# Kernel optimization log

Measured on AMD Instinct MI355X. Metric: run time of the kernel, lower is better.

Reference implementation:

```python
import jax, jax.numpy as jnp
import numpy as np

B, T, TC, C, CC, H = 2, 2048, 512, 1024, 512, 16
D = C // H  # head dim = 64


def setup_inputs() -> dict:
    key = jax.random.key(0)
    ks = jax.random.split(key, 18)
    w = lambda k, i, o: (jax.random.normal(k, (i, o), jnp.float32) / np.sqrt(i).astype(np.float32))
    return {
        "x": jax.random.normal(ks[0], (B, T, C), jnp.float32),
        "cross_input": jax.random.normal(ks[1], (B, TC, CC), jnp.float32),
        "Wk": w(ks[2], C, C),  "bk": jnp.zeros((C,), jnp.float32),
        "Wq": w(ks[3], C, C),  "bq": jnp.zeros((C,), jnp.float32),
        "Wv": w(ks[4], C, C),  "bv": jnp.zeros((C,), jnp.float32),
        "Wck": w(ks[5], CC, C), "bck": jnp.zeros((C,), jnp.float32),
        "Wcq": w(ks[6], C, C),  "bcq": jnp.zeros((C,), jnp.float32),
        "Wcv": w(ks[7], CC, C), "bcv": jnp.zeros((C,), jnp.float32),
        "Wp": w(ks[8], C, C),   "bp": jnp.zeros((C,), jnp.float32),
    }


def _heads(t):
    # [B, L, C] -> [B, H, L, D]
    b, l, _ = t.shape
    return t.reshape(b, l, H, D).transpose(0, 2, 1, 3)


def reference(x, cross_input, Wk, bk, Wq, bq, Wv, bv, Wck, bck, Wcq, bcq, Wcv, bcv, Wp, bp):
    scale = np.float32(1.0 / np.sqrt(D))
    q = _heads(x @ Wq + bq)
    k = _heads(x @ Wk + bk)
    v = _heads(x @ Wv + bv)
    # causal self-attention with materialized scores (faithful to original)
    att = jnp.einsum("bhqd,bhkd->bhqk", q, k) * scale
    causal = jnp.tril(jnp.ones((T, T), bool))
    att = jnp.where(causal[None, None], att, -jnp.inf)
    y = jnp.einsum("bhqk,bhkd->bhqd", jax.nn.softmax(att, axis=-1), v)
    # cross-attention (no mask)
    qc = _heads(x @ Wcq + bcq)
    kc = _heads(cross_input @ Wck + bck)
    vc = _heads(cross_input @ Wcv + bcv)
    attc = jnp.einsum("bhqd,bhkd->bhqk", qc, kc) * scale
    y = y + jnp.einsum("bhqk,bhkd->bhqd", jax.nn.softmax(attc, axis=-1), vc)
    # merge heads + output projection (dropout prob = 0 -> identity)
    y = y.transpose(0, 2, 1, 3).reshape(x.shape[0], T, C)
    return y @ Wp + bp
```

## Files before the change

kernel.cpp:

```cpp
#include <hip/hip_runtime.h>
#include <hip/hip_bf16.h>
#include <type_traits>

typedef __bf16 bf16;
typedef __bf16 bf16x8 __attribute__((ext_vector_type(8)));
typedef float floatx4 __attribute__((ext_vector_type(4)));

#if __has_builtin(__builtin_amdgcn_exp2f)
#define EXP2(x) __builtin_amdgcn_exp2f(x)
#else
#define EXP2(x) exp2f(x)
#endif

__device__ __forceinline__ void glds16(const bf16* g, bf16* l) {
  __builtin_amdgcn_global_load_lds((const __attribute__((address_space(1))) void*)g,
                                   (__attribute__((address_space(3))) void*)l, 16, 0, 0);
}

__device__ __forceinline__ unsigned pack_bf16(float a, float b) {
  unsigned short ua = __builtin_bit_cast(unsigned short, (bf16)a);
  unsigned short ub = __builtin_bit_cast(unsigned short, (bf16)b);
  return (unsigned)ua | ((unsigned)ub << 16);
}

struct PrepArgs {
  const float* x; const float* xc;
  bf16* xbf; bf16* xcbf;
  const float* b4[4];
  const float* bc[2];
  float* bias4; float* biasc;
  const float* W[7];
  bf16* WT[7];
};

__global__ __launch_bounds__(256) void prep_kernel(PrepArgs a) {
  __shared__ bf16 tsh[32][33];
  const int bx = blockIdx.x, tid = threadIdx.x;
  if (bx < 4096) {
    int i = bx * 256 + tid;
    float4 f = ((const float4*)a.x)[i];
    bf16 t[4] = {(bf16)f.x, (bf16)f.y, (bf16)f.z, (bf16)f.w};
    *(uint2*)&a.xbf[(long)i * 4] = *(const uint2*)t;
  } else if (bx < 4608) {
    int i = (bx - 4096) * 256 + tid;
    float4 f = ((const float4*)a.xc)[i];
    bf16 t[4] = {(bf16)f.x, (bf16)f.y, (bf16)f.z, (bf16)f.w};
    *(uint2*)&a.xcbf[(long)i * 4] = *(const uint2*)t;
  } else if (bx < 4632) {
    int lb = bx - 4608;
    if (lb < 16) { int i = lb * 256 + tid; a.bias4[i] = a.b4[i >> 10][i & 1023]; }
    else         { int i = (lb - 16) * 256 + tid; a.biasc[i] = a.bc[i >> 10][i & 1023]; }
  } else {
    int t = bx - 4632, w, R, bxw, byw;
    if (t < 5120) { w = t >> 10; R = 1024; int l = t & 1023; bxw = l & 31; byw = l >> 5; }
    else { int t2 = t - 5120; w = 5 + (t2 >> 9); R = 512; int l = t2 & 511; bxw = l & 31; byw = l >> 5; }
    const float* in = a.W[w];
    bf16* out = a.WT[w];
    int tx = tid & 31, ty = tid >> 5;
    int c = bxw * 32 + tx;
#pragma unroll
    for (int i = 0; i < 4; i++) {
      int r = byw * 32 + ty + i * 8;
      tsh[ty + i * 8][tx] = (bf16)in[(long)r * 1024 + c];
    }
    __syncthreads();
    int oc = byw * 32 + tx;
#pragma unroll
    for (int i = 0; i < 4; i++) {
      int orr = bxw * 32 + ty + i * 8;
      out[(long)orr * R + oc] = tsh[tx][ty + i * 8];
    }
  }
}

template <typename OutT>
__global__ __launch_bounds__(256, 3) void gemm128(const bf16* __restrict__ A,
                                                  const bf16* __restrict__ Bt,
                                                  const float* __restrict__ bias,
                                                  OutT* __restrict__ C,
                                                  int M, int N, int K, int ldc,
                                                  bf16* __restrict__ Vt,
                                                  int vcol0, int vcol1, int Lt, int tok_shift) {
  __shared__ alignas(16) bf16 As[128 * 32];
  __shared__ alignas(16) bf16 Bs[128 * 32];
  const int tid = threadIdx.x, wave = tid >> 6, lane = tid & 63;
  const int l16 = lane & 15, l4 = lane >> 4;
  const int wm = wave & 1, wn = wave >> 1;
  const int n0 = blockIdx.x * 128, m0 = blockIdx.y * 128;
  const int lrow = lane >> 2, lch = (lane & 3) * 8;

  floatx4 acc[4][4];
#pragma unroll
  for (int mt = 0; mt < 4; mt++)
#pragma unroll
    for (int nt = 0; nt < 4; nt++) acc[mt][nt] = (floatx4){0.f, 0.f, 0.f, 0.f};

  const bf16* Ag = A + (long)(m0 + wave * 32 + lrow) * K + lch;
  const bf16* Bg = Bt + (long)(n0 + wave * 32 + lrow) * K + lch;
  bf16* Al = &As[(wave * 32) * 32];
  bf16* Bl = &Bs[(wave * 32) * 32];

  for (int k0 = 0; k0 < K; k0 += 32) {
    __syncthreads();
    glds16(Ag + k0, Al);
    glds16(Ag + k0 + (long)16 * K, Al + 16 * 32);
    glds16(Bg + k0, Bl);
    glds16(Bg + k0 + (long)16 * K, Bl + 16 * 32);
    __syncthreads();
    bf16x8 a[4], b[4];
#pragma unroll
    for (int mt = 0; mt < 4; mt++) a[mt] = *(const bf16x8*)&As[(wm * 64 + mt * 16 + l16) * 32 + l4 * 8];
#pragma unroll
    for (int nt = 0; nt < 4; nt++) b[nt] = *(const bf16x8*)&Bs[(wn * 64 + nt * 16 + l16) * 32 + l4 * 8];
#pragma unroll
    for (int mt = 0; mt < 4; mt++)
#pragma unroll
      for (int nt = 0; nt < 4; nt++)
        acc[mt][nt] = __builtin_amdgcn_mfma_f32_16x16x32_bf16(a[mt], b[nt], acc[mt][nt], 0, 0, 0);
  }

  const bool vpath = (vcol0 >= 0) && (n0 >= vcol0) && (n0 < vcol1);
  if (!vpath) {
    const int coladj = (vcol0 >= 0 && n0 >= vcol1) ? (vcol1 - vcol0) : 0;
#pragma unroll
    for (int nt = 0; nt < 4; nt++) {
      int col = n0 + wn * 64 + nt * 16 + l16;
      float bv = bias[col];
#pragma unroll
      for (int mt = 0; mt < 4; mt++)
#pragma unroll
        for (int r = 0; r < 4; r++) {
          int row = m0 + wm * 64 + mt * 16 + l4 * 4 + r;
          float v = acc[mt][nt][r] + bv;
          if constexpr (std::is_same_v<OutT, float>) C[(long)row * ldc + col - coladj] = v;
          else                                       C[(long)row * ldc + col - coladj] = (bf16)v;
        }
    }
  } else {
#pragma unroll
    for (int nt = 0; nt < 4; nt++) {
      int col = n0 + wn * 64 + nt * 16 + l16;
      int c = col - vcol0, hh = c >> 6, dd = c & 63;
      float bv = bias[col];
#pragma unroll
      for (int mt = 0; mt < 4; mt++) {
        int t0 = m0 + wm * 64 + mt * 16 + l4 * 4;
        int bb = t0 >> tok_shift, t = t0 & ((1 << tok_shift) - 1);
        bf16 tmp[4];
#pragma unroll
        for (int r = 0; r < 4; r++) tmp[r] = (bf16)(acc[mt][nt][r] + bv);
        *(uint2*)&Vt[(((long)bb * 16 + hh) * 64 + dd) * Lt + t] = *(const uint2*)tmp;
      }
    }
  }
}

__global__ __launch_bounds__(256, 2) void attn_kernel(const bf16* __restrict__ QKQc,
                                                      const bf16* __restrict__ VtB,
                                                      const bf16* __restrict__ KcB,
                                                      const bf16* __restrict__ VctB,
                                                      bf16* __restrict__ Y) {
  __shared__ float2 Mbuf[4][4][16];
  __shared__ alignas(16) bf16 U[4 * 64 * 72];
  const int tid = threadIdx.x, w = tid >> 6, lane = tid & 63;
  const int l16 = lane & 15, l4 = lane >> 4;
  const int bh = blockIdx.x, h = bh & 15, b = bh >> 4;
  const int qt = 31 - (int)blockIdx.y;
  const int q0 = qt * 64;
  const int wk = w * 32;
  bf16* Pw = U + w * (64 * 48);
  const float NEG = -1e30f;

  float o_self[16];

  for (int phase = 0; phase < 2; phase++) {
    const bf16 *Qb, *Kb, *Vtb;
    int kstr, vtstr, nkt;
    if (phase == 0) {
      Qb = QKQc + (long)b * 2048 * 3072 + h * 64;
      Kb = Qb + 1024;                              kstr = 3072;
      Vtb = VtB + ((long)b * 16 + h) * 64 * 2048;  vtstr = 2048;
      nkt = (qt + 2) >> 1;
    } else {
      Qb = QKQc + (long)b * 2048 * 3072 + h * 64 + 2048;
      Kb = KcB + (long)b * 512 * 1024 + h * 64;    kstr = 1024;
      Vtb = VctB + ((long)b * 16 + h) * 64 * 512;  vtstr = 512;
      nkt = 4;
    }

    __syncthreads();

    bf16x8 qf[4][2];
#pragma unroll
    for (int qtt = 0; qtt < 4; qtt++) {
      const bf16* qp = Qb + (long)(q0 + qtt * 16 + l16) * 3072 + l4 * 8;
#pragma unroll
      for (int ds = 0; ds < 2; ds++) {
        bf16x8 v = *(const bf16x8*)(qp + ds * 32);
#pragma unroll
        for (int j = 0; j < 8; j++) v[j] = (bf16)((float)v[j] * 0.18033688f);
        qf[qtt][ds] = v;
      }
    }

    float m_i[4], l_i[4];
#pragma unroll
    for (int qtt = 0; qtt < 4; qtt++) { m_i[qtt] = NEG; l_i[qtt] = 0.f; }
    floatx4 oacc[4][4];
#pragma unroll
    for (int mtd = 0; mtd < 4; mtd++)
#pragma unroll
      for (int qtt = 0; qtt < 4; qtt++) oacc[mtd][qtt] = (floatx4){0.f, 0.f, 0.f, 0.f};

    bf16x8 kc[2][2], kn[2][2];
#pragma unroll
    for (int mt = 0; mt < 2; mt++)
#pragma unroll
      for (int ds = 0; ds < 2; ds++)
        kc[mt][ds] = *(const bf16x8*)(Kb + (long)(wk + mt * 16 + l16) * kstr + ds * 32 + l4 * 8);

    for (int kt = 0; kt < nkt; kt++) {
      const int kbase = kt * 128 + wk;
      bf16x8 vc[4];
#pragma unroll
      for (int mtd = 0; mtd < 4; mtd++)
        vc[mtd] = *(const bf16x8*)(Vtb + (long)(mtd * 16 + l16) * vtstr + kbase + l4 * 8);

      floatx4 sacc[2][4];
#pragma unroll
      for (int mt = 0; mt < 2; mt++)
#pragma unroll
        for (int qtt = 0; qtt < 4; qtt++) sacc[mt][qtt] = (floatx4){0.f, 0.f, 0.f, 0.f};
#pragma unroll
      for (int ds = 0; ds < 2; ds++)
#pragma unroll
        for (int mt = 0; mt < 2; mt++)
#pragma unroll
          for (int qtt = 0; qtt < 4; qtt++)
            sacc[mt][qtt] = __builtin_amdgcn_mfma_f32_16x16x32_bf16(kc[mt][ds], qf[qtt][ds], sacc[mt][qtt], 0, 0, 0);

      if (kt + 1 < nkt) {
        const int nb = kbase + 128;
#pragma unroll
        for (int mt = 0; mt < 2; mt++)
#pragma unroll
          for (int ds = 0; ds < 2; ds++)
            kn[mt][ds] = *(const bf16x8*)(Kb + (long)(nb + mt * 16 + l16) * kstr + ds * 32 + l4 * 8);
      }

      if (phase == 0 && kt == nkt - 1) {
#pragma unroll
        for (int mt = 0; mt < 2; mt++) {
          int keyb = kbase + mt * 16 + l4 * 4;
#pragma unroll
          for (int qtt = 0; qtt < 4; qtt++) {
            int q = q0 + qtt * 16 + l16;
#pragma unroll
            for (int r = 0; r < 4; r++)
              if (keyb + r > q) sacc[mt][qtt][r] = NEG;
          }
        }
      }

      float alpha[4];
      unsigned pd[4][2][2];
      int changed = 0;
#pragma unroll
      for (int qtt = 0; qtt < 4; qtt++) {
        float mx = fmaxf(fmaxf(fmaxf(sacc[0][qtt][0], sacc[0][qtt][1]), fmaxf(sacc[0][qtt][2], sacc[0][qtt][3])),
                         fmaxf(fmaxf(sacc[1][qtt][0], sacc[1][qtt][1]), fmaxf(sacc[1][qtt][2], sacc[1][qtt][3])));
        mx = fmaxf(mx, __shfl_xor(mx, 16));
        mx = fmaxf(mx, __shfl_xor(mx, 32));
        mx = fmaxf(mx, m_i[qtt]);
        alpha[qtt] = EXP2(m_i[qtt] - mx);
        changed |= (mx > m_i[qtt]) ? 1 : 0;
        m_i[qtt] = mx;
        float rs = 0.f;
#pragma unroll
        for (int mt = 0; mt < 2; mt++) {
          float p0 = EXP2(sacc[mt][qtt][0] - mx), p1 = EXP2(sacc[mt][qtt][1] - mx);
          float p2 = EXP2(sacc[mt][qtt][2] - mx), p3 = EXP2(sacc[mt][qtt][3] - mx);
          rs += (p0 + p1) + (p2 + p3);
          pd[qtt][mt][0] = pack_bf16(p0, p1);
          pd[qtt][mt][1] = pack_bf16(p2, p3);
        }
        rs += __shfl_xor(rs, 16);
        rs += __shfl_xor(rs, 32);
        l_i[qtt] = l_i[qtt] * alpha[qtt] + rs;
      }
      if (__any(changed)) {
#pragma unroll
        for (int mtd = 0; mtd < 4; mtd++)
#pragma unroll
          for (int qtt = 0; qtt < 4; qtt++)
#pragma unroll
            for (int r = 0; r < 4; r++) oacc[mtd][qtt][r] *= alpha[qtt];
      }

#pragma unroll
      for (int qtt = 0; qtt < 4; qtt++)
#pragma unroll
        for (int mt = 0; mt < 2; mt++) {
          uint2 u = {pd[qtt][mt][0], pd[qtt][mt][1]};
          *(uint2*)&Pw[(qtt * 16 + l16) * 48 + mt * 16 + l4 * 4] = u;
        }
#pragma unroll
      for (int qtt = 0; qtt < 4; qtt++) {
        bf16x8 pf = *(const bf16x8*)&Pw[(qtt * 16 + l16) * 48 + l4 * 8];
#pragma unroll
        for (int mtd = 0; mtd < 4; mtd++)
          oacc[mtd][qtt] = __builtin_amdgcn_mfma_f32_16x16x32_bf16(vc[mtd], pf, oacc[mtd][qtt], 0, 0, 0);
      }
#pragma unroll
      for (int mt = 0; mt < 2; mt++)
#pragma unroll
        for (int ds = 0; ds < 2; ds++) kc[mt][ds] = kn[mt][ds];
    }

    if (l4 == 0) {
#pragma unroll
      for (int qtt = 0; qtt < 4; qtt++) Mbuf[w][qtt][l16] = make_float2(m_i[qtt], l_i[qtt]);
    }
    __syncthreads();
    float myscale[4], denom[4];
#pragma unroll
    for (int qtt = 0; qtt < 4; qtt++) {
      float2 s0 = Mbuf[0][qtt][l16], s1 = Mbuf[1][qtt][l16];
      float2 s2 = Mbuf[2][qtt][l16], s3 = Mbuf[3][qtt][l16];
      float M = fmaxf(fmaxf(s0.x, s1.x), fmaxf(s2.x, s3.x));
      denom[qtt] = EXP2(s0.x - M) * s0.y + EXP2(s1.x - M) * s1.y +
                   EXP2(s2.x - M) * s2.y + EXP2(s3.x - M) * s3.y;
      myscale[qtt] = EXP2(m_i[qtt] - M);
    }
#pragma unroll
    for (int qtt = 0; qtt < 4; qtt++)
#pragma unroll
      for (int mtd = 0; mtd < 4; mtd++) {
        float s = myscale[qtt];
        uint2 u = {pack_bf16(oacc[mtd][qtt][0] * s, oacc[mtd][qtt][1] * s),
                   pack_bf16(oacc[mtd][qtt][2] * s, oacc[mtd][qtt][3] * s)};
        *(uint2*)&U[((w * 64) + qtt * 16 + l16) * 72 + mtd * 16 + l4 * 4] = u;
      }
    __syncthreads();
    float sum[16];
#pragma unroll
    for (int j = 0; j < 16; j++) sum[j] = 0.f;
#pragma unroll
    for (int s = 0; s < 4; s++) {
      bf16x8 c0 = *(const bf16x8*)&U[((s * 64) + w * 16 + l16) * 72 + l4 * 16];
      bf16x8 c1 = *(const bf16x8*)&U[((s * 64) + w * 16 + l16) * 72 + l4 * 16 + 8];
#pragma unroll
      for (int j = 0; j < 8; j++) { sum[j] += (float)c0[j]; sum[8 + j] += (float)c1[j]; }
    }
    float invd = 1.0f / denom[w];
    if (phase == 0) {
#pragma unroll
      for (int j = 0; j < 16; j++) o_self[j] = sum[j] * invd;
    } else {
      long row = (long)b * 2048 + q0 + w * 16 + l16;
      bf16 out[16];
#pragma unroll
      for (int j = 0; j < 16; j++) out[j] = (bf16)(o_self[j] + sum[j] * invd);
      *(bf16x8*)&Y[row * 1024 + h * 64 + l4 * 16] = *(const bf16x8*)&out[0];
      *(bf16x8*)&Y[row * 1024 + h * 64 + l4 * 16 + 8] = *(const bf16x8*)&out[8];
    }
  }
}

extern "C" void kernel_launch(void* const* d_in, const int* in_sizes, int n_in,
                              void* d_out, int out_size, void* d_ws, size_t ws_size,
                              hipStream_t stream) {
  const float* x   = (const float*)d_in[0];
  const float* xc  = (const float*)d_in[1];
  const float* Wk  = (const float*)d_in[2];  const float* bk  = (const float*)d_in[3];
  const float* Wq  = (const float*)d_in[4];  const float* bq  = (const float*)d_in[5];
  const float* Wv  = (const float*)d_in[6];  const float* bv  = (const float*)d_in[7];
  const float* Wck = (const float*)d_in[8];  const float* bck = (const float*)d_in[9];
  const float* Wcq = (const float*)d_in[10]; const float* bcq = (const float*)d_in[11];
  const float* Wcv = (const float*)d_in[12]; const float* bcv = (const float*)d_in[13];
  const float* Wp  = (const float*)d_in[14]; const float* bp  = (const float*)d_in[15];

  char* ws = (char*)d_ws;
  const size_t MB = 1ull << 20;
  bf16*  WT_all = (bf16*)(ws + 0);
  bf16*  WC_all = (bf16*)(ws + 8 * MB);
  bf16*  WpT    = (bf16*)(ws + 10 * MB);
  bf16*  xbf    = (bf16*)(ws + 12 * MB);
  bf16*  Yb     = xbf;
  bf16*  xcbf   = (bf16*)(ws + 20 * MB);
  float* bias4  = (float*)(ws + 21 * MB);
  float* biasc  = (float*)(ws + 21 * MB + 65536);
  bf16*  QKQc   = (bf16*)(ws + 22 * MB);
  bf16*  VtB    = (bf16*)(ws + 46 * MB);
  bf16*  KcB    = (bf16*)(ws + 54 * MB);
  bf16*  VctB   = (bf16*)(ws + 56 * MB);

  PrepArgs pa;
  pa.x = x; pa.xc = xc; pa.xbf = xbf; pa.xcbf = xcbf;
  pa.b4[0] = bq; pa.b4[1] = bk; pa.b4[2] = bv; pa.b4[3] = bcq;
  pa.bc[0] = bck; pa.bc[1] = bcv;
  pa.bias4 = bias4; pa.biasc = biasc;
  pa.W[0] = Wq;  pa.WT[0] = WT_all + 0ll * 1024 * 1024;
  pa.W[1] = Wk;  pa.WT[1] = WT_all + 1ll * 1024 * 1024;
  pa.W[2] = Wv;  pa.WT[2] = WT_all + 2ll * 1024 * 1024;
  pa.W[3] = Wcq; pa.WT[3] = WT_all + 3ll * 1024 * 1024;
  pa.W[4] = Wp;  pa.WT[4] = WpT;
  pa.W[5] = Wck; pa.WT[5] = WC_all + 0ll * 1024 * 512;
  pa.W[6] = Wcv; pa.WT[6] = WC_all + 1ll * 1024 * 512;
  prep_kernel<<<10776, 256, 0, stream>>>(pa);

  gemm128<bf16><<<dim3(32, 32), 256, 0, stream>>>(xbf, WT_all, bias4, QKQc,
                                                  4096, 4096, 1024, 3072,
                                                  VtB, 2048, 3072, 2048, 11);
  gemm128<bf16><<<dim3(16, 8), 256, 0, stream>>>(xcbf, WC_all, biasc, KcB,
                                                 1024, 2048, 512, 1024,
                                                 VctB, 1024, 2048, 512, 9);

  attn_kernel<<<dim3(32, 32), 256, 0, stream>>>(QKQc, VtB, KcB, VctB, Yb);

  gemm128<float><<<dim3(8, 32), 256, 0, stream>>>(Yb, WpT, bp, (float*)d_out,
                                                  4096, 1024, 1024, 1024,
                                                  nullptr, -1, -1, 0, 0);
}
```

Baseline: 260.9 us.

## Fold Q scaling into projection GEMM and feed P directly to MFMA

Moves the softmax scale of the query columns (self and cross Q) into the QKV projection GEMM epilogue, so the attention kernel no longer rescales Q after loading it. When the 16x16x16 bf16 MFMA builtin is available, the P matrix is used straight from registers as the B operand, with V loaded in matching 4-element fragments. This removes the LDS round-trip for P. Occupancy hint for attention is raised to 3 blocks per CU, which may constrain registers and cause spills. The smaller-K MFMA doubles the instruction count for the PV product.

```diff
diff --git a/kernel.cpp b/kernel.cpp
--- a/kernel.cpp
+++ b/kernel.cpp
@@ -5,12 +5,21 @@
 typedef __bf16 bf16;
 typedef __bf16 bf16x8 __attribute__((ext_vector_type(8)));
 typedef float floatx4 __attribute__((ext_vector_type(4)));
+typedef short short4v __attribute__((ext_vector_type(4)));
+
+#if __has_builtin(__builtin_amdgcn_mfma_f32_16x16x16bf16_1k)
+#define DIRECT_PV 1
+#else
+#define DIRECT_PV 0
+#endif
 
 #if __has_builtin(__builtin_amdgcn_exp2f)
 #define EXP2(x) __builtin_amdgcn_exp2f(x)
 #else
 #define EXP2(x) exp2f(x)
 #endif
+
+#define QSCALE 0.18033688011112043f
 
 __device__ __forceinline__ void glds16(const bf16* g, bf16* l) {
   __builtin_amdgcn_global_load_lds((const __attribute__((address_space(1))) void*)g,
@@ -80,7 +89,8 @@
                                                   OutT* __restrict__ C,
                                                   int M, int N, int K, int ldc,
                                                   bf16* __restrict__ Vt,
-                                                  int vcol0, int vcol1, int Lt, int tok_shift) {
+                                                  int vcol0, int vcol1, int Lt, int tok_shift,
+                                                  int qflag) {
   __shared__ alignas(16) bf16 As[128 * 32];
   __shared__ alignas(16) bf16 Bs[128 * 32];
   const int tid = threadIdx.x, wave = tid >> 6, lane = tid & 63;
@@ -126,12 +136,13 @@
     for (int nt = 0; nt < 4; nt++) {
       int col = n0 + wn * 64 + nt * 16 + l16;
       float bv = bias[col];
+      float sc = (qflag && (col < 1024 || col >= 3072)) ? QSCALE : 1.0f;
 #pragma unroll
       for (int mt = 0; mt < 4; mt++)
 #pragma unroll
         for (int r = 0; r < 4; r++) {
           int row = m0 + wm * 64 + mt * 16 + l4 * 4 + r;
-          float v = acc[mt][nt][r] + bv;
+          float v = (acc[mt][nt][r] + bv) * sc;
           if constexpr (std::is_same_v<OutT, float>) C[(long)row * ldc + col - coladj] = v;
           else                                       C[(long)row * ldc + col - coladj] = (bf16)v;
         }
@@ -155,7 +166,7 @@
   }
 }
 
-__global__ __launch_bounds__(256, 2) void attn_kernel(const bf16* __restrict__ QKQc,
+__global__ __launch_bounds__(256, 3) void attn_kernel(const bf16* __restrict__ QKQc,
                                                       const bf16* __restrict__ VtB,
                                                       const bf16* __restrict__ KcB,
                                                       const bf16* __restrict__ VctB,
@@ -168,8 +179,10 @@
   const int qt = 31 - (int)blockIdx.y;
   const int q0 = qt * 64;
   const int wk = w * 32;
-  bf16* Pw = U + w * (64 * 48);
   const float NEG = -1e30f;
+#if !DIRECT_PV
+  bf16* Pw = U + w * (64 * 44);
+#endif
 
   float o_self[16];
 
@@ -195,12 +208,7 @@
     for (int qtt = 0; qtt < 4; qtt++) {
       const bf16* qp = Qb + (long)(q0 + qtt * 16 + l16) * 3072 + l4 * 8;
 #pragma unroll
-      for (int ds = 0; ds < 2; ds++) {
-        bf16x8 v = *(const bf16x8*)(qp + ds * 32);
-#pragma unroll
-        for (int j = 0; j < 8; j++) v[j] = (bf16)((float)v[j] * 0.18033688f);
-        qf[qtt][ds] = v;
-      }
+      for (int ds = 0; ds < 2; ds++) qf[qtt][ds] = *(const bf16x8*)(qp + ds * 32);
     }
 
     float m_i[4], l_i[4];
@@ -221,10 +229,19 @@
 
     for (int kt = 0; kt < nkt; kt++) {
       const int kbase = kt * 128 + wk;
+#if DIRECT_PV
+      uint2 vf[4][2];
+#pragma unroll
+      for (int mtd = 0; mtd < 4; mtd++)
+#pragma unroll
+        for (int mt = 0; mt < 2; mt++)
+          vf[mtd][mt] = *(const uint2*)(Vtb + (long)(mtd * 16 + l16) * vtstr + kbase + mt * 16 + l4 * 4);
+#else
       bf16x8 vc[4];
 #pragma unroll
       for (int mtd = 0; mtd < 4; mtd++)
         vc[mtd] = *(const bf16x8*)(Vtb + (long)(mtd * 16 + l16) * vtstr + kbase + l4 * 8);
+#endif
 
       floatx4 sacc[2][4];
 #pragma unroll
@@ -263,7 +280,7 @@
       }
 
       float alpha[4];
-      unsigned pd[4][2][2];
+      uint2 pd[4][2];
       int changed = 0;
 #pragma unroll
       for (int qtt = 0; qtt < 4; qtt++) {
@@ -281,8 +298,8 @@
           float p0 = EXP2(sacc[mt][qtt][0] - mx), p1 = EXP2(sacc[mt][qtt][1] - mx);
           float p2 = EXP2(sacc[mt][qtt][2] - mx), p3 = EXP2(sacc[mt][qtt][3] - mx);
           rs += (p0 + p1) + (p2 + p3);
-          pd[qtt][mt][0] = pack_bf16(p0, p1);
-          pd[qtt][mt][1] = pack_bf16(p2, p3);
+          pd[qtt][mt].x = pack_bf16(p0, p1);
+          pd[qtt][mt].y = pack_bf16(p2, p3);
         }
         rs += __shfl_xor(rs, 16);
         rs += __shfl_xor(rs, 32);
@@ -297,20 +314,31 @@
             for (int r = 0; r < 4; r++) oacc[mtd][qtt][r] *= alpha[qtt];
       }
 
+#if DIRECT_PV
 #pragma unroll
       for (int qtt = 0; qtt < 4; qtt++)
 #pragma unroll
         for (int mt = 0; mt < 2; mt++) {
-          uint2 u = {pd[qtt][mt][0], pd[qtt][mt][1]};
-          *(uint2*)&Pw[(qtt * 16 + l16) * 48 + mt * 16 + l4 * 4] = u;
+          short4v pf = __builtin_bit_cast(short4v, pd[qtt][mt]);
+#pragma unroll
+          for (int mtd = 0; mtd < 4; mtd++)
+            oacc[mtd][qtt] = __builtin_amdgcn_mfma_f32_16x16x16bf16_1k(
+                __builtin_bit_cast(short4v, vf[mtd][mt]), pf, oacc[mtd][qtt], 0, 0, 0);
         }
+#else
+#pragma unroll
+      for (int qtt = 0; qtt < 4; qtt++)
+#pragma unroll
+        for (int mt = 0; mt < 2; mt++)
+          *(uint2*)&Pw[(qtt * 16 + l16) * 44 + mt * 16 + l4 * 4] = pd[qtt][mt];
 #pragma unroll
       for (int qtt = 0; qtt < 4; qtt++) {
-        bf16x8 pf = *(const bf16x8*)&Pw[(qtt * 16 + l16) * 48 + l4 * 8];
+        bf16x8 pf = *(const bf16x8*)&Pw[(qtt * 16 + l16) * 44 + l4 * 8];
 #pragma unroll
         for (int mtd = 0; mtd < 4; mtd++)
           oacc[mtd][qtt] = __builtin_amdgcn_mfma_f32_16x16x32_bf16(vc[mtd], pf, oacc[mtd][qtt], 0, 0, 0);
       }
+#endif
 #pragma unroll
       for (int mt = 0; mt < 2; mt++)
 #pragma unroll
@@ -411,14 +439,14 @@
 
   gemm128<bf16><<<dim3(32, 32), 256, 0, stream>>>(xbf, WT_all, bias4, QKQc,
                                                   4096, 4096, 1024, 3072,
-                                                  VtB, 2048, 3072, 2048, 11);
+                                                  VtB, 2048, 3072, 2048, 11, 1);
   gemm128<bf16><<<dim3(16, 8), 256, 0, stream>>>(xcbf, WC_all, biasc, KcB,
                                                  1024, 2048, 512, 1024,
-                                                 VctB, 1024, 2048, 512, 9);
+                                                 VctB, 1024, 2048, 512, 9, 0);
 
   attn_kernel<<<dim3(32, 32), 256, 0, stream>>>(QKQc, VtB, KcB, VctB, Yb);
 
   gemm128<float><<<dim3(8, 32), 256, 0, stream>>>(Yb, WpT, bp, (float*)d_out,
                                                   4096, 1024, 1024, 1024,
-                                                  nullptr, -1, -1, 0, 0);
-}
+                                                  nullptr, -1, -1, 0, 0, 0);
+}
```

New measurement: 386.0 us. +48.0%, slower.

## Cut attention register pressure to raise occupancy and fold Q scaling into GEMM

Applied to the files above, without the earlier changes.

Fold the softmax scale into the QKV projection epilogue for the Q and cross-Q columns, so the attention kernel no longer rescales Q. In the attention kernel, drop the K register prefetch, write probabilities straight to LDS instead of staging them in registers, and keep the self-attention partial output in LDS rather than registers. Launch bounds go from 2 to 3 blocks per CU. The aim is to cut VGPR use so more waves run, at the cost of losing the K prefetch overlap, extra LDS traffic, and one more bf16 rounding of the self-attention output.

```diff
diff --git a/kernel.cpp b/kernel.cpp
--- a/kernel.cpp
+++ b/kernel.cpp
@@ -11,6 +11,8 @@
 #else
 #define EXP2(x) exp2f(x)
 #endif
+
+#define QSCALE 0.18033688011112043f
 
 __device__ __forceinline__ void glds16(const bf16* g, bf16* l) {
   __builtin_amdgcn_global_load_lds((const __attribute__((address_space(1))) void*)g,
@@ -80,7 +82,8 @@
                                                   OutT* __restrict__ C,
                                                   int M, int N, int K, int ldc,
                                                   bf16* __restrict__ Vt,
-                                                  int vcol0, int vcol1, int Lt, int tok_shift) {
+                                                  int vcol0, int vcol1, int Lt, int tok_shift,
+                                                  int qflag) {
   __shared__ alignas(16) bf16 As[128 * 32];
   __shared__ alignas(16) bf16 Bs[128 * 32];
   const int tid = threadIdx.x, wave = tid >> 6, lane = tid & 63;
@@ -126,12 +129,13 @@
     for (int nt = 0; nt < 4; nt++) {
       int col = n0 + wn * 64 + nt * 16 + l16;
       float bv = bias[col];
+      float sc = (qflag && (col < 1024 || col >= 3072)) ? QSCALE : 1.0f;
 #pragma unroll
       for (int mt = 0; mt < 4; mt++)
 #pragma unroll
         for (int r = 0; r < 4; r++) {
           int row = m0 + wm * 64 + mt * 16 + l4 * 4 + r;
-          float v = acc[mt][nt][r] + bv;
+          float v = (acc[mt][nt][r] + bv) * sc;
           if constexpr (std::is_same_v<OutT, float>) C[(long)row * ldc + col - coladj] = v;
           else                                       C[(long)row * ldc + col - coladj] = (bf16)v;
         }
@@ -155,23 +159,22 @@
   }
 }
 
-__global__ __launch_bounds__(256, 2) void attn_kernel(const bf16* __restrict__ QKQc,
+__global__ __launch_bounds__(256, 3) void attn_kernel(const bf16* __restrict__ QKQc,
                                                       const bf16* __restrict__ VtB,
                                                       const bf16* __restrict__ KcB,
                                                       const bf16* __restrict__ VctB,
                                                       bf16* __restrict__ Y) {
   __shared__ float2 Mbuf[4][4][16];
   __shared__ alignas(16) bf16 U[4 * 64 * 72];
+  __shared__ alignas(16) bf16 Osf[64 * 72];
   const int tid = threadIdx.x, w = tid >> 6, lane = tid & 63;
   const int l16 = lane & 15, l4 = lane >> 4;
   const int bh = blockIdx.x, h = bh & 15, b = bh >> 4;
   const int qt = 31 - (int)blockIdx.y;
   const int q0 = qt * 64;
   const int wk = w * 32;
-  bf16* Pw = U + w * (64 * 48);
   const float NEG = -1e30f;
-
-  float o_self[16];
+  bf16* Pw = U + w * (64 * 44);
 
   for (int phase = 0; phase < 2; phase++) {
     const bf16 *Qb, *Kb, *Vtb;
@@ -195,12 +198,7 @@
     for (int qtt = 0; qtt < 4; qtt++) {
       const bf16* qp = Qb + (long)(q0 + qtt * 16 + l16) * 3072 + l4 * 8;
 #pragma unroll
-      for (int ds = 0; ds < 2; ds++) {
-        bf16x8 v = *(const bf16x8*)(qp + ds * 32);
-#pragma unroll
-        for (int j = 0; j < 8; j++) v[j] = (bf16)((float)v[j] * 0.18033688f);
-        qf[qtt][ds] = v;
-      }
+      for (int ds = 0; ds < 2; ds++) qf[qtt][ds] = *(const bf16x8*)(qp + ds * 32);
     }
 
     float m_i[4], l_i[4];
@@ -212,15 +210,14 @@
 #pragma unroll
       for (int qtt = 0; qtt < 4; qtt++) oacc[mtd][qtt] = (floatx4){0.f, 0.f, 0.f, 0.f};
 
-    bf16x8 kc[2][2], kn[2][2];
-#pragma unroll
-    for (int mt = 0; mt < 2; mt++)
-#pragma unroll
-      for (int ds = 0; ds < 2; ds++)
-        kc[mt][ds] = *(const bf16x8*)(Kb + (long)(wk + mt * 16 + l16) * kstr + ds * 32 + l4 * 8);
-
     for (int kt = 0; kt < nkt; kt++) {
       const int kbase = kt * 128 + wk;
+      bf16x8 kc[2][2];
+#pragma unroll
+      for (int mt = 0; mt < 2; mt++)
+#pragma unroll
+        for (int ds = 0; ds < 2; ds++)
+          kc[mt][ds] = *(const bf16x8*)(Kb + (long)(kbase + mt * 16 + l16) * kstr + ds * 32 + l4 * 8);
       bf16x8 vc[4];
 #pragma unroll
       for (int mtd = 0; mtd < 4; mtd++)
@@ -238,15 +235,6 @@
 #pragma unroll
           for (int qtt = 0; qtt < 4; qtt++)
             sacc[mt][qtt] = __builtin_amdgcn_mfma_f32_16x16x32_bf16(kc[mt][ds], qf[qtt][ds], sacc[mt][qtt], 0, 0, 0);
-
-      if (kt + 1 < nkt) {
-        const int nb = kbase + 128;
-#pragma unroll
-        for (int mt = 0; mt < 2; mt++)
-#pragma unroll
-          for (int ds = 0; ds < 2; ds++)
-            kn[mt][ds] = *(const bf16x8*)(Kb + (long)(nb + mt * 16 + l16) * kstr + ds * 32 + l4 * 8);
-      }
 
       if (phase == 0 && kt == nkt - 1) {
 #pragma unroll
@@ -263,7 +251,6 @@
       }
 
       float alpha[4];
-      unsigned pd[4][2][2];
       int changed = 0;
 #pragma unroll
       for (int qtt = 0; qtt < 4; qtt++) {
@@ -281,8 +268,8 @@
           float p0 = EXP2(sacc[mt][qtt][0] - mx), p1 = EXP2(sacc[mt][qtt][1] - mx);
           float p2 = EXP2(sacc[mt][qtt][2] - mx), p3 = EXP2(sacc[mt][qtt][3] - mx);
           rs += (p0 + p1) + (p2 + p3);
-          pd[qtt][mt][0] = pack_bf16(p0, p1);
-          pd[qtt][mt][1] = pack_bf16(p2, p3);
+          uint2 u = {pack_bf16(p0, p1), pack_bf16(p2, p3)};
+          *(uint2*)&Pw[(qtt * 16 + l16) * 44 + mt * 16 + l4 * 4] = u;
         }
         rs += __shfl_xor(rs, 16);
         rs += __shfl_xor(rs, 32);
@@ -298,23 +285,12 @@
       }
 
 #pragma unroll
-      for (int qtt = 0; qtt < 4; qtt++)
-#pragma unroll
-        for (int mt = 0; mt < 2; mt++) {
-          uint2 u = {pd[qtt][mt][0], pd[qtt][mt][1]};
-          *(uint2*)&Pw[(qtt * 16 + l16) * 48 + mt * 16 + l4 * 4] = u;
-        }
-#pragma unroll
       for (int qtt = 0; qtt < 4; qtt++) {
-        bf16x8 pf = *(const bf16x8*)&Pw[(qtt * 16 + l16) * 48 + l4 * 8];
+        bf16x8 pf = *(const bf16x8*)&Pw[(qtt * 16 + l16) * 44 + l4 * 8];
 #pragma unroll
         for (int mtd = 0; mtd < 4; mtd++)
           oacc[mtd][qtt] = __builtin_amdgcn_mfma_f32_16x16x32_bf16(vc[mtd], pf, oacc[mtd][qtt], 0, 0, 0);
       }
-#pragma unroll
-      for (int mt = 0; mt < 2; mt++)
-#pragma unroll
-        for (int ds = 0; ds < 2; ds++) kc[mt][ds] = kn[mt][ds];
     }
 
     if (l4 == 0) {
@@ -354,13 +330,21 @@
     }
     float invd = 1.0f / denom[w];
     if (phase == 0) {
-#pragma unroll
-      for (int j = 0; j < 16; j++) o_self[j] = sum[j] * invd;
+      bf16 t[16];
+#pragma unroll
+      for (int j = 0; j < 16; j++) t[j] = (bf16)(sum[j] * invd);
+      *(bf16x8*)&Osf[(w * 16 + l16) * 72 + l4 * 16] = *(const bf16x8*)&t[0];
+      *(bf16x8*)&Osf[(w * 16 + l16) * 72 + l4 * 16 + 8] = *(const bf16x8*)&t[8];
     } else {
+      bf16x8 p0 = *(const bf16x8*)&Osf[(w * 16 + l16) * 72 + l4 * 16];
+      bf16x8 p1 = *(const bf16x8*)&Osf[(w * 16 + l16) * 72 + l4 * 16 + 8];
       long row = (long)b * 2048 + q0 + w * 16 + l16;
       bf16 out[16];
 #pragma unroll
-      for (int j = 0; j < 16; j++) out[j] = (bf16)(o_self[j] + sum[j] * invd);
+      for (int j = 0; j < 8; j++) {
+        out[j] = (bf16)((float)p0[j] + sum[j] * invd);
+        out[8 + j] = (bf16)((float)p1[j] + sum[8 + j] * invd);
+      }
       *(bf16x8*)&Y[row * 1024 + h * 64 + l4 * 16] = *(const bf16x8*)&out[0];
       *(bf16x8*)&Y[row * 1024 + h * 64 + l4 * 16 + 8] = *(const bf16x8*)&out[8];
     }
@@ -411,14 +395,14 @@
 
   gemm128<bf16><<<dim3(32, 32), 256, 0, stream>>>(xbf, WT_all, bias4, QKQc,
                                                   4096, 4096, 1024, 3072,
-                                                  VtB, 2048, 3072, 2048, 11);
+                                                  VtB, 2048, 3072, 2048, 11, 1);
   gemm128<bf16><<<dim3(16, 8), 256, 0, stream>>>(xcbf, WC_all, biasc, KcB,
                                                  1024, 2048, 512, 1024,
-                                                 VctB, 1024, 2048, 512, 9);
+                                                 VctB, 1024, 2048, 512, 9, 0);
 
   attn_kernel<<<dim3(32, 32), 256, 0, stream>>>(QKQc, VtB, KcB, VctB, Yb);
 
   gemm128<float><<<dim3(8, 32), 256, 0, stream>>>(Yb, WpT, bp, (float*)d_out,
                                                   4096, 1024, 1024, 1024,
-                                                  nullptr, -1, -1, 0, 0);
-}
+                                                  nullptr, -1, -1, 0, 0, 0);
+}
```

Measured after the change: 317.6 us. 1.22x slower.
